# Kernel optimization log

Hardware: AMD Instinct MI355X
Metric: run time of the kernel (lower is better)

Reference implementation:

```python
import jax, jax.numpy as jnp
import numpy as np

NUM_HEADS = 16
EMBED_DIM = 1024
INPUT_DIM = 1024
B, S = 4, 1024
MASK_VAL = -1e30  # fp32 branch of the original code


def setup_inputs() -> dict:
    key = jax.random.key(0)
    k1, k2, k3, k4 = jax.random.split(key, 4)
    x = jax.random.normal(k1, (B, S, INPUT_DIM), dtype=jnp.float32)
    mask = jax.random.randint(k2, (B, S), 0, 2, dtype=jnp.int32)
    # xavier_uniform-like init
    lim_qkv = float(np.sqrt(6.0 / (INPUT_DIM + 3 * EMBED_DIM)))
    lim_out = float(np.sqrt(6.0 / (EMBED_DIM + EMBED_DIM)))
    w_qkv = jax.random.uniform(k3, (3 * EMBED_DIM, INPUT_DIM), jnp.float32, -lim_qkv, lim_qkv)
    b_qkv = jnp.zeros((3 * EMBED_DIM,), jnp.float32)
    w_out = jax.random.uniform(k4, (EMBED_DIM, EMBED_DIM), jnp.float32, -lim_out, lim_out)
    b_out = jnp.zeros((EMBED_DIM,), jnp.float32)
    return {"x": x, "mask": mask, "w_qkv": w_qkv, "b_qkv": b_qkv,
            "w_out": w_out, "b_out": b_out}


def reference(x, mask, w_qkv, b_qkv, w_out, b_out):
    Bz, Sl, _ = x.shape
    Dh = EMBED_DIM // NUM_HEADS
    qkv = x @ w_qkv.T + b_qkv                       # (B,S,3E)
    q, k, v = jnp.split(qkv, 3, axis=-1)
    q = q.reshape(Bz, Sl, NUM_HEADS, Dh).transpose(0, 2, 1, 3)  # (B,H,S,Dh)
    k = k.reshape(Bz, Sl, NUM_HEADS, Dh).transpose(0, 2, 1, 3)
    v = v.reshape(Bz, Sl, NUM_HEADS, Dh).transpose(0, 2, 1, 3)
    energy = jnp.einsum('bhqd,bhkd->bhqk', q, k) / jnp.sqrt(jnp.float32(Dh))
    # Faithful reproduction of the original (buggy-looking) mask semantics:
    # positions with (k <= q) & (q < L_i) & (k < L_i) get filled with -1e30.
    L = mask.sum(axis=-1)                            # (B,)
    idx = jnp.arange(Sl)
    tri = idx[:, None] >= idx[None, :]               # (S,S): k <= q
    valid = idx[None, :] < L[:, None]                # (B,S)
    cond = tri[None, None] & valid[:, None, :, None] & valid[:, None, None, :]
    energy = jnp.where(cond, MASK_VAL, energy)
    attn = jax.nn.softmax(energy, axis=-1)           # (B,H,S,S)
    out = jnp.einsum('bhqk,bhkd->bhqd', attn, v)     # (B,H,S,Dh)
    out = out.transpose(0, 2, 1, 3).reshape(Bz, Sl, EMBED_DIM)
    return out @ w_out.T + b_out
```

## Files before the change

### kernel.cpp

```cpp
#include <hip/hip_runtime.h>


#define NHEADS 16
#define DHEAD  64
#define EDIM   1024
#define SLEN   1024
#define BATCH  4

typedef short bf16x8 __attribute__((ext_vector_type(8)));
typedef float f32x4  __attribute__((ext_vector_type(4)));
typedef float f32x16 __attribute__((ext_vector_type(16)));

#define MFMA_BF16(a,b,c) __builtin_amdgcn_mfma_f32_16x16x32_bf16((a),(b),(c),0,0,0)
#define MFMA32(a,b,c)    __builtin_amdgcn_mfma_f32_32x32x16_bf16((a),(b),(c),0,0,0)

typedef const __attribute__((address_space(1))) void gvoid_t;
typedef __attribute__((address_space(3))) void lvoid_t;

__device__ __forceinline__ unsigned short f2bf(float x) {
  union { float f; unsigned int u; } v; v.f = x;
  unsigned int r = v.u + 0x7fffu + ((v.u >> 16) & 1u);
  return (unsigned short)(r >> 16);
}

__device__ __forceinline__ unsigned pack2(float lo, float hi) {
  return (unsigned)f2bf(lo) | ((unsigned)f2bf(hi) << 16);
}

__device__ __forceinline__ void gl2lds16(const void* g, void* l) {
  __builtin_amdgcn_global_load_lds((gvoid_t*)g, (lvoid_t*)l, 16, 0, 0);
}

__global__ __launch_bounds__(256) void prep_cast(
    const float* __restrict__ x, const float* __restrict__ wq,
    const float* __restrict__ wo,
    unsigned short* __restrict__ xb, unsigned short* __restrict__ wqb,
    unsigned short* __restrict__ wob) {
  int i = blockIdx.x * 256 + threadIdx.x;
  const int NX  = BATCH * SLEN * EDIM / 4;
  const int NW1 = 3 * EDIM * EDIM / 4;
  const float4* src; unsigned short* dst; int j;
  if (i < NX)           { src = (const float4*)x;  dst = xb;  j = i; }
  else if (i < NX+NW1)  { src = (const float4*)wq; dst = wqb; j = i - NX; }
  else                  { src = (const float4*)wo; dst = wob; j = i - NX - NW1; }
  float4 v = src[j];
  ushort4 o;
  o.x = f2bf(v.x); o.y = f2bf(v.y); o.z = f2bf(v.z); o.w = f2bf(v.w);
  ((ushort4*)dst)[j] = o;
}

__global__ __launch_bounds__(256) void mask_sum(const int* __restrict__ mask,
                                                int* __restrict__ L) {
  int b = blockIdx.x;
  int t = threadIdx.x;
  int s = 0;
  for (int i = t; i < SLEN; i += 256) s += mask[b * SLEN + i];
  #pragma unroll
  for (int m = 1; m < 64; m <<= 1) s += __shfl_xor(s, m);
  __shared__ int part[4];
  if ((t & 63) == 0) part[t >> 6] = s;
  __syncthreads();
  if (t == 0) L[b] = part[0] + part[1] + part[2] + part[3];
}

template<int EPI>
__global__ __launch_bounds__(256) void gemm_bt(
    const unsigned short* __restrict__ A, const unsigned short* __restrict__ B,
    int M, int N, int K,
    const float* __restrict__ bias,
    float* __restrict__ outf,
    unsigned short* __restrict__ qb, unsigned short* __restrict__ kb,
    unsigned short* __restrict__ vb) {
  __shared__ __align__(16) unsigned short lds_a[128 * 32];
  __shared__ __align__(16) unsigned short lds_b[128 * 32];
  const int tid = threadIdx.x;
  const int w = tid >> 6, l = tid & 63;
  const int g = l >> 4, ln = l & 15;
  const int ntile = N >> 7;
  const int tm = blockIdx.x / ntile, tn = blockIdx.x % ntile;
  const int mBase = tm << 7, nBase = tn << 7;
  const int wr = w >> 1, wc = w & 1;

  f32x4 zz = {0.f, 0.f, 0.f, 0.f};
  f32x4 acc[4][4];
  #pragma unroll
  for (int m = 0; m < 4; ++m)
    #pragma unroll
    for (int n = 0; n < 4; ++n) acc[m][n] = zz;

  const int u0 = tid, u1 = tid + 256;
  const int r0 = u0 >> 2, c0 = (u0 & 3) << 3;
  const int r1 = u1 >> 2, c1 = (u1 & 3) << 3;
  const unsigned short* Ab = A + mBase * K;
  const unsigned short* Bb = B + nBase * K;
  unsigned short* da0 = &lds_a[(w * 64) * 8];
  unsigned short* da1 = &lds_a[(256 + w * 64) * 8];
  unsigned short* db0 = &lds_b[(w * 64) * 8];
  unsigned short* db1 = &lds_b[(256 + w * 64) * 8];

  for (int k0 = 0; k0 < K; k0 += 32) {
    gl2lds16(Ab + r0 * K + k0 + c0, da0);
    gl2lds16(Ab + r1 * K + k0 + c1, da1);
    gl2lds16(Bb + r0 * K + k0 + c0, db0);
    gl2lds16(Bb + r1 * K + k0 + c1, db1);
    __syncthreads();
    bf16x8 af[4], bfr[4];
    #pragma unroll
    for (int m = 0; m < 4; ++m)
      af[m] = *(const bf16x8*)&lds_a[(wr * 64 + m * 16 + ln) * 32 + g * 8];
    #pragma unroll
    for (int n = 0; n < 4; ++n)
      bfr[n] = *(const bf16x8*)&lds_b[(wc * 64 + n * 16 + ln) * 32 + g * 8];
    #pragma unroll
    for (int m = 0; m < 4; ++m)
      #pragma unroll
      for (int n = 0; n < 4; ++n)
        acc[m][n] = MFMA_BF16(af[m], bfr[n], acc[m][n]);
    __syncthreads();
  }

  #pragma unroll
  for (int m = 0; m < 4; ++m) {
    const int rowb = mBase + wr * 64 + m * 16 + g * 4;
    #pragma unroll
    for (int n = 0; n < 4; ++n) {
      const int col = nBase + wc * 64 + n * 16 + ln;
      const float bv = bias[col];
      #pragma unroll
      for (int r = 0; r < 4; ++r) {
        const float vv = acc[m][n][r] + bv;
        const int row = rowb + r;
        if (EPI == 0) {
          const int part = col >> 10;
          const int c = col & 1023;
          const int hh = c >> 6, d = c & 63;
          const int bb = row >> 10, s = row & 1023;
          const int bh = bb * NHEADS + hh;
          const unsigned short hv = f2bf(vv);
          if (part == 0)      qb[(bh * SLEN + s) * DHEAD + d] = hv;
          else if (part == 1) kb[(bh * SLEN + s) * DHEAD + d] = hv;
          else                vb[(bh * DHEAD + d) * SLEN + s] = hv;
        } else {
          outf[row * N + col] = vv;
        }
      }
    }
  }
}

__global__ __launch_bounds__(256) void attn(
    const unsigned short* __restrict__ qb, const unsigned short* __restrict__ kb,
    const unsigned short* __restrict__ vb, const int* __restrict__ Lp,
    unsigned short* __restrict__ yb) {
  const int bid = blockIdx.x;
  const int lid = (bid & 7) * 256 + (bid >> 3);
  const int bh = lid >> 5, qw = lid & 31;
  const int b = bh >> 4, h = bh & 15;
  const int L = Lp[b];
  const int tid = threadIdx.x;
  const int w = tid >> 6, l = tid & 63;
  const int l31 = l & 31, hi = l >> 5;
  const int q = qw * 32 + l31;

  const unsigned short* qp = qb + (size_t)bh * SLEN * DHEAD;
  const unsigned short* kp = kb + (size_t)bh * SLEN * DHEAD;
  const unsigned short* vp = vb + (size_t)bh * DHEAD * SLEN;

  bf16x8 qf[4];
  #pragma unroll
  for (int c = 0; c < 4; ++c)
    qf[c] = *(const bf16x8*)&qp[q * DHEAD + c * 16 + hi * 8];

  f32x16 o0 = {}; f32x16 o1 = {};
  float mrow = -__builtin_inff(), lrow = 0.f;
  const bool qv = q < L;
  const float C = 0.18033688011112042f;

  const bool allQ  = (qw * 32 + 31) < L;
  const bool noneQ = (qw * 32) >= L;
  const int tstart = (allQ && L < SLEN) ? qw : 0;
  const int tlo = tstart + ((w - tstart) & 3);

  const int tp = tlo < 32 ? tlo : 31;
  bf16x8 kcur[4];
  #pragma unroll
  for (int c = 0; c < 4; ++c)
    kcur[c] = *(const bf16x8*)&kp[(tp * 32 + l31) * DHEAD + c * 16 + hi * 8];

  for (int t = tlo; t < 32; t += 4) {
    const int kb0 = t * 32;
    const int tn = (t + 4 < 32) ? (t + 4) : t;
    bf16x8 knxt[4];
    #pragma unroll
    for (int c = 0; c < 4; ++c)
      knxt[c] = *(const bf16x8*)&kp[(tn * 32 + l31) * DHEAD + c * 16 + hi * 8];
    bf16x8 vf0[2], vf1[2];
    #pragma unroll
    for (int kc = 0; kc < 2; ++kc) {
      vf0[kc] = *(const bf16x8*)&vp[l31 * SLEN + kb0 + kc * 16 + hi * 8];
      vf1[kc] = *(const bf16x8*)&vp[(32 + l31) * SLEN + kb0 + kc * 16 + hi * 8];
    }

    f32x16 e = {};
    __builtin_amdgcn_s_setprio(1);
    #pragma unroll
    for (int c = 0; c < 4; ++c) e = MFMA32(kcur[c], qf[c], e);
    __builtin_amdgcn_s_setprio(0);

    const bool domask = (!noneQ) && (t <= qw);
    float pm = -__builtin_inff();
    if (domask) {
      #pragma unroll
      for (int r = 0; r < 16; ++r) {
        const int key = kb0 + (r & 3) + 8 * (r >> 2) + 4 * hi;
        float s = e[r] * C;
        if (qv && (key <= q)) s = -1e30f;
        e[r] = s;
        pm = fmaxf(pm, s);
      }
    } else {
      #pragma unroll
      for (int r = 0; r < 16; ++r) {
        const float s = e[r] * C;
        e[r] = s;
        pm = fmaxf(pm, s);
      }
    }
    pm = fmaxf(pm, __shfl_xor(pm, 32));

    const bool need = !__all(pm <= mrow + 8.0f);
    if (need) {
      const float mn = fmaxf(mrow, pm);
      const float a = exp2f(mrow - mn);
      #pragma unroll
      for (int r = 0; r < 16; ++r) { o0[r] *= a; o1[r] *= a; }
      lrow *= a;
      mrow = mn;
    }
    float sum = 0.f;
    #pragma unroll
    for (int r = 0; r < 16; ++r) {
      const float pe = exp2f(e[r] - mrow);
      e[r] = pe; sum += pe;
    }
    sum += __shfl_xor(sum, 32);
    lrow += sum;

    bf16x8 pbf[2];
    #pragma unroll
    for (int kc = 0; kc < 2; ++kc) {
      const unsigned wA = pack2(e[8*kc+0], e[8*kc+1]);
      const unsigned wB = pack2(e[8*kc+2], e[8*kc+3]);
      const unsigned wC = pack2(e[8*kc+4], e[8*kc+5]);
      const unsigned wD = pack2(e[8*kc+6], e[8*kc+7]);
      const unsigned pA = __shfl_xor(wA, 32);
      const unsigned pB = __shfl_xor(wB, 32);
      const unsigned pC = __shfl_xor(wC, 32);
      const unsigned pD = __shfl_xor(wD, 32);
      union { unsigned u[4]; bf16x8 v; } pk;
      pk.u[0] = hi ? pC : wA;
      pk.u[1] = hi ? pD : wB;
      pk.u[2] = hi ? wC : pA;
      pk.u[3] = hi ? wD : pB;
      pbf[kc] = pk.v;
    }

    __builtin_amdgcn_s_setprio(1);
    #pragma unroll
    for (int kc = 0; kc < 2; ++kc) {
      o0 = MFMA32(vf0[kc], pbf[kc], o0);
      o1 = MFMA32(vf1[kc], pbf[kc], o1);
    }
    __builtin_amdgcn_s_setprio(0);

    #pragma unroll
    for (int c = 0; c < 4; ++c) kcur[c] = knxt[c];
  }

  __shared__ float mls[4][2][32];
  __shared__ __align__(16) float obuf[2][32][65];
  if (hi == 0) { mls[w][0][l31] = mrow; mls[w][1][l31] = lrow; }
  __syncthreads();
  const float m0 = mls[0][0][l31], m1 = mls[1][0][l31];
  const float m2 = mls[2][0][l31], m3 = mls[3][0][l31];
  const float mstar = fmaxf(fmaxf(m0, m1), fmaxf(m2, m3));
  const float denom = mls[0][1][l31] * exp2f(m0 - mstar)
                    + mls[1][1][l31] * exp2f(m1 - mstar)
                    + mls[2][1][l31] * exp2f(m2 - mstar)
                    + mls[3][1][l31] * exp2f(m3 - mstar);
  const float sw = exp2f(mrow - mstar) / denom;
  #pragma unroll
  for (int r = 0; r < 16; ++r) { o0[r] *= sw; o1[r] *= sw; }
  if (w >= 2) {
    #pragma unroll
    for (int r = 0; r < 16; ++r) {
      const int d = (r & 3) + 8 * (r >> 2) + 4 * hi;
      obuf[w - 2][l31][d]      = o0[r];
      obuf[w - 2][l31][d + 32] = o1[r];
    }
  }
  __syncthreads();
  if (w < 2) {
    #pragma unroll
    for (int r = 0; r < 16; ++r) {
      const int d = (r & 3) + 8 * (r >> 2) + 4 * hi;
      o0[r] += obuf[w][l31][d];
      o1[r] += obuf[w][l31][d + 32];
    }
  }
  __syncthreads();
  if (w == 1) {
    #pragma unroll
    for (int r = 0; r < 16; ++r) {
      const int d = (r & 3) + 8 * (r >> 2) + 4 * hi;
      obuf[0][l31][d]      = o0[r];
      obuf[0][l31][d + 32] = o1[r];
    }
  }
  __syncthreads();
  if (w == 0) {
    #pragma unroll
    for (int r = 0; r < 16; ++r) {
      const int d = (r & 3) + 8 * (r >> 2) + 4 * hi;
      o0[r] += obuf[0][l31][d];
      o1[r] += obuf[0][l31][d + 32];
    }
    unsigned short* yrow = yb + (size_t)(b * SLEN + q) * EDIM + h * DHEAD;
    #pragma unroll
    for (int rq = 0; rq < 4; ++rq) {
      ushort4 s0, s1;
      s0.x = f2bf(o0[4*rq+0]); s0.y = f2bf(o0[4*rq+1]);
      s0.z = f2bf(o0[4*rq+2]); s0.w = f2bf(o0[4*rq+3]);
      s1.x = f2bf(o1[4*rq+0]); s1.y = f2bf(o1[4*rq+1]);
      s1.z = f2bf(o1[4*rq+2]); s1.w = f2bf(o1[4*rq+3]);
      *(ushort4*)&yrow[8*rq + 4*hi]      = s0;
      *(ushort4*)&yrow[32 + 8*rq + 4*hi] = s1;
    }
  }
}

extern "C" void kernel_launch(void* const* d_in, const int* in_sizes, int n_in,
                              void* d_out, int out_size, void* d_ws, size_t ws_size,
                              hipStream_t stream) {
  const float* x    = (const float*)d_in[0];
  const int*   mask = (const int*)d_in[1];
  const float* wqkv = (const float*)d_in[2];
  const float* bqkv = (const float*)d_in[3];
  const float* wout = (const float*)d_in[4];
  const float* bout = (const float*)d_in[5];
  float* out = (float*)d_out;

  char* ws = (char*)d_ws;
  const size_t SZ_X   = (size_t)BATCH * SLEN * EDIM * 2;
  const size_t SZ_WQ  = (size_t)3 * EDIM * EDIM * 2;
  const size_t SZ_WO  = (size_t)EDIM * EDIM * 2;
  const size_t SZ_QKV = (size_t)BATCH * NHEADS * SLEN * DHEAD * 2;

  unsigned short* xb   = (unsigned short*)ws;               ws += SZ_X;
  unsigned short* wqb  = (unsigned short*)ws;               ws += SZ_WQ;
  unsigned short* wob  = (unsigned short*)ws;               ws += SZ_WO;
  unsigned short* qbuf = (unsigned short*)ws;               ws += SZ_QKV;
  unsigned short* kbuf = (unsigned short*)ws;               ws += SZ_QKV;
  unsigned short* vbuf = (unsigned short*)ws;               ws += SZ_QKV;
  unsigned short* ybuf = (unsigned short*)ws;               ws += SZ_X;
  int* Lbuf = (int*)ws;

  prep_cast<<<8192, 256, 0, stream>>>(x, wqkv, wout, xb, wqb, wob);
  mask_sum<<<BATCH, 256, 0, stream>>>(mask, Lbuf);
  gemm_bt<0><<<(4096 / 128) * (3072 / 128), 256, 0, stream>>>(
      xb, wqb, 4096, 3072, 1024, bqkv, nullptr, qbuf, kbuf, vbuf);
  attn<<<BATCH * NHEADS * (SLEN / 32), 256, 0, stream>>>(qbuf, kbuf, vbuf, Lbuf, ybuf);
  gemm_bt<1><<<(4096 / 128) * (1024 / 128), 256, 0, stream>>>(
      ybuf, wob, 4096, 1024, 1024, bout, out, nullptr, nullptr, nullptr);
}
```

Before: 230.4 us.

## Process two 32-query tiles per attention block to reuse K/V loads

Each attention workgroup now handles 64 queries as two 32-row sub-tiles (A and B), sharing each loaded K and V fragment across both sub-tiles' QK and PV MFMAs. The grid halves, and global K/V traffic per query is halved. The cost is doubled accumulator and register state per wave, larger shared-memory reduction buffers, and a combined start tile that may add iterations for the lower sub-tile. Occupancy may drop because of register pressure.

```diff
diff --git a/kernel.cpp b/kernel.cpp
--- a/kernel.cpp
+++ b/kernel.cpp
@@ -153,33 +153,39 @@
     const unsigned short* __restrict__ vb, const int* __restrict__ Lp,
     unsigned short* __restrict__ yb) {
   const int bid = blockIdx.x;
-  const int lid = (bid & 7) * 256 + (bid >> 3);
-  const int bh = lid >> 5, qw = lid & 31;
+  const int lid = (bid & 7) * 128 + (bid >> 3);
+  const int bh = lid >> 4, qp = lid & 15;
   const int b = bh >> 4, h = bh & 15;
   const int L = Lp[b];
   const int tid = threadIdx.x;
   const int w = tid >> 6, l = tid & 63;
   const int l31 = l & 31, hi = l >> 5;
-  const int q = qw * 32 + l31;
-
-  const unsigned short* qp = qb + (size_t)bh * SLEN * DHEAD;
-  const unsigned short* kp = kb + (size_t)bh * SLEN * DHEAD;
-  const unsigned short* vp = vb + (size_t)bh * DHEAD * SLEN;
-
-  bf16x8 qf[4];
+  const int q0 = qp * 64;
+  const int qA = q0 + l31, qB = q0 + 32 + l31;
+  const int qwA = 2 * qp, qwB = 2 * qp + 1;
+
+  const unsigned short* qp_ = qb + (size_t)bh * SLEN * DHEAD;
+  const unsigned short* kp  = kb + (size_t)bh * SLEN * DHEAD;
+  const unsigned short* vp  = vb + (size_t)bh * DHEAD * SLEN;
+
+  bf16x8 qfA[4], qfB[4];
   #pragma unroll
-  for (int c = 0; c < 4; ++c)
-    qf[c] = *(const bf16x8*)&qp[q * DHEAD + c * 16 + hi * 8];
-
-  f32x16 o0 = {}; f32x16 o1 = {};
-  float mrow = -__builtin_inff(), lrow = 0.f;
-  const bool qv = q < L;
+  for (int c = 0; c < 4; ++c) {
+    qfA[c] = *(const bf16x8*)&qp_[qA * DHEAD + c * 16 + hi * 8];
+    qfB[c] = *(const bf16x8*)&qp_[qB * DHEAD + c * 16 + hi * 8];
+  }
+
+  f32x16 o0A = {}, o1A = {}, o0B = {}, o1B = {};
+  float mA = -__builtin_inff(), lsA = 0.f;
+  float mB = -__builtin_inff(), lsB = 0.f;
   const float C = 0.18033688011112042f;
 
-  const bool allQ  = (qw * 32 + 31) < L;
-  const bool noneQ = (qw * 32) >= L;
-  const int tstart = (allQ && L < SLEN) ? qw : 0;
-  const int tlo = tstart + ((w - tstart) & 3);
+  const bool noneA = q0 >= L,        noneB = (q0 + 32) >= L;
+  const bool allA  = (q0 + 31) < L,  allB  = (q0 + 63) < L;
+  const int tsA = (allA && L < SLEN) ? qwA : 0;
+  const int tsB = (allB && L < SLEN) ? qwB : 0;
+  const int ts  = tsA < tsB ? tsA : tsB;
+  const int tlo = ts + ((w - ts) & 3);
 
   const int tp = tlo < 32 ? tlo : 31;
   bf16x8 kcur[4];
@@ -187,6 +193,67 @@
   for (int c = 0; c < 4; ++c)
     kcur[c] = *(const bf16x8*)&kp[(tp * 32 + l31) * DHEAD + c * 16 + hi * 8];
 
+#define SM_PV(SUF)                                                          \
+  {                                                                         \
+    const bool domask = (!none##SUF) && (t <= qw##SUF);                     \
+    float pm = -__builtin_inff();                                           \
+    if (domask) {                                                           \
+      _Pragma("unroll")                                                     \
+      for (int r = 0; r < 16; ++r) {                                        \
+        const int key = kb0 + (r & 3) + 8 * (r >> 2) + 4 * hi;              \
+        float s = e##SUF[r] * C;                                            \
+        if ((q##SUF < L) && (key <= q##SUF)) s = -1e30f;                    \
+        e##SUF[r] = s; pm = fmaxf(pm, s);                                   \
+      }                                                                     \
+    } else {                                                                \
+      _Pragma("unroll")                                                     \
+      for (int r = 0; r < 16; ++r) {                                        \
+        const float s = e##SUF[r] * C; e##SUF[r] = s; pm = fmaxf(pm, s);    \
+      }                                                                     \
+    }                                                                       \
+    pm = fmaxf(pm, __shfl_xor(pm, 32));                                     \
+    const bool need = !__all(pm <= m##SUF + 8.0f);                          \
+    if (need) {                                                             \
+      const float mn = fmaxf(m##SUF, pm);                                   \
+      const float a = exp2f(m##SUF - mn);                                   \
+      _Pragma("unroll")                                                     \
+      for (int r = 0; r < 16; ++r) { o0##SUF[r] *= a; o1##SUF[r] *= a; }    \
+      ls##SUF *= a; m##SUF = mn;                                            \
+    }                                                                       \
+    float sum = 0.f;                                                        \
+    _Pragma("unroll")                                                       \
+    for (int r = 0; r < 16; ++r) {                                          \
+      const float pe = exp2f(e##SUF[r] - m##SUF);                           \
+      e##SUF[r] = pe; sum += pe;                                            \
+    }                                                                       \
+    sum += __shfl_xor(sum, 32);                                             \
+    ls##SUF += sum;                                                         \
+    bf16x8 pbf[2];                                                          \
+    _Pragma("unroll")                                                       \
+    for (int kc = 0; kc < 2; ++kc) {                                        \
+      const unsigned wA_ = pack2(e##SUF[8*kc+0], e##SUF[8*kc+1]);           \
+      const unsigned wB_ = pack2(e##SUF[8*kc+2], e##SUF[8*kc+3]);           \
+      const unsigned wC_ = pack2(e##SUF[8*kc+4], e##SUF[8*kc+5]);           \
+      const unsigned wD_ = pack2(e##SUF[8*kc+6], e##SUF[8*kc+7]);           \
+      const unsigned pA_ = __shfl_xor(wA_, 32);                             \
+      const unsigned pB_ = __shfl_xor(wB_, 32);                             \
+      const unsigned pC_ = __shfl_xor(wC_, 32);                             \
+      const unsigned pD_ = __shfl_xor(wD_, 32);                             \
+      union { unsigned u[4]; bf16x8 v; } pk;                                \
+      pk.u[0] = hi ? pC_ : wA_;                                             \
+      pk.u[1] = hi ? pD_ : wB_;                                             \
+      pk.u[2] = hi ? wC_ : pA_;                                             \
+      pk.u[3] = hi ? wD_ : pB_;                                             \
+      pbf[kc] = pk.v;                                                       \
+    }                                                                       \
+    __builtin_amdgcn_s_setprio(1);                                          \
+    o0##SUF = MFMA32(vf0[0], pbf[0], o0##SUF);                              \
+    o1##SUF = MFMA32(vf1[0], pbf[0], o1##SUF);                              \
+    o0##SUF = MFMA32(vf0[1], pbf[1], o0##SUF);                              \
+    o1##SUF = MFMA32(vf1[1], pbf[1], o1##SUF);                              \
+    __builtin_amdgcn_s_setprio(0);                                          \
+  }
+
   for (int t = tlo; t < 32; t += 4) {
     const int kb0 = t * 32;
     const int tn = (t + 4 < 32) ? (t + 4) : t;
@@ -201,102 +268,59 @@
       vf1[kc] = *(const bf16x8*)&vp[(32 + l31) * SLEN + kb0 + kc * 16 + hi * 8];
     }
 
-    f32x16 e = {};
+    f32x16 eA = {}, eB = {};
     __builtin_amdgcn_s_setprio(1);
     #pragma unroll
-    for (int c = 0; c < 4; ++c) e = MFMA32(kcur[c], qf[c], e);
+    for (int c = 0; c < 4; ++c) eA = MFMA32(kcur[c], qfA[c], eA);
+    #pragma unroll
+    for (int c = 0; c < 4; ++c) eB = MFMA32(kcur[c], qfB[c], eB);
     __builtin_amdgcn_s_setprio(0);
 
-    const bool domask = (!noneQ) && (t <= qw);
-    float pm = -__builtin_inff();
-    if (domask) {
-      #pragma unroll
-      for (int r = 0; r < 16; ++r) {
-        const int key = kb0 + (r & 3) + 8 * (r >> 2) + 4 * hi;
-        float s = e[r] * C;
-        if (qv && (key <= q)) s = -1e30f;
-        e[r] = s;
-        pm = fmaxf(pm, s);
-      }
-    } else {
-      #pragma unroll
-      for (int r = 0; r < 16; ++r) {
-        const float s = e[r] * C;
-        e[r] = s;
-        pm = fmaxf(pm, s);
-      }
-    }
-    pm = fmaxf(pm, __shfl_xor(pm, 32));
-
-    const bool need = !__all(pm <= mrow + 8.0f);
-    if (need) {
-      const float mn = fmaxf(mrow, pm);
-      const float a = exp2f(mrow - mn);
-      #pragma unroll
-      for (int r = 0; r < 16; ++r) { o0[r] *= a; o1[r] *= a; }
-      lrow *= a;
-      mrow = mn;
-    }
-    float sum = 0.f;
-    #pragma unroll
-    for (int r = 0; r < 16; ++r) {
-      const float pe = exp2f(e[r] - mrow);
-      e[r] = pe; sum += pe;
-    }
-    sum += __shfl_xor(sum, 32);
-    lrow += sum;
-
-    bf16x8 pbf[2];
-    #pragma unroll
-    for (int kc = 0; kc < 2; ++kc) {
-      const unsigned wA = pack2(e[8*kc+0], e[8*kc+1]);
-      const unsigned wB = pack2(e[8*kc+2], e[8*kc+3]);
-      const unsigned wC = pack2(e[8*kc+4], e[8*kc+5]);
-      const unsigned wD = pack2(e[8*kc+6], e[8*kc+7]);
-      const unsigned pA = __shfl_xor(wA, 32);
-      const unsigned pB = __shfl_xor(wB, 32);
-      const unsigned pC = __shfl_xor(wC, 32);
-      const unsigned pD = __shfl_xor(wD, 32);
-      union { unsigned u[4]; bf16x8 v; } pk;
-      pk.u[0] = hi ? pC : wA;
-      pk.u[1] = hi ? pD : wB;
-      pk.u[2] = hi ? wC : pA;
-      pk.u[3] = hi ? wD : pB;
-      pbf[kc] = pk.v;
-    }
-
-    __builtin_amdgcn_s_setprio(1);
-    #pragma unroll
-    for (int kc = 0; kc < 2; ++kc) {
-      o0 = MFMA32(vf0[kc], pbf[kc], o0);
-      o1 = MFMA32(vf1[kc], pbf[kc], o1);
-    }
-    __builtin_amdgcn_s_setprio(0);
+    if (t >= tsA) SM_PV(A)
+    if (t >= tsB) SM_PV(B)
 
     #pragma unroll
     for (int c = 0; c < 4; ++c) kcur[c] = knxt[c];
   }
-
-  __shared__ float mls[4][2][32];
-  __shared__ __align__(16) float obuf[2][32][65];
-  if (hi == 0) { mls[w][0][l31] = mrow; mls[w][1][l31] = lrow; }
+#undef SM_PV
+
+  __shared__ float mlsA[4][2][32], mlsB[4][2][32];
+  __shared__ __align__(16) float obufA[2][32][65], obufB[2][32][65];
+  if (hi == 0) {
+    mlsA[w][0][l31] = mA; mlsA[w][1][l31] = lsA;
+    mlsB[w][0][l31] = mB; mlsB[w][1][l31] = lsB;
+  }
   __syncthreads();
-  const float m0 = mls[0][0][l31], m1 = mls[1][0][l31];
-  const float m2 = mls[2][0][l31], m3 = mls[3][0][l31];
-  const float mstar = fmaxf(fmaxf(m0, m1), fmaxf(m2, m3));
-  const float denom = mls[0][1][l31] * exp2f(m0 - mstar)
-                    + mls[1][1][l31] * exp2f(m1 - mstar)
-                    + mls[2][1][l31] * exp2f(m2 - mstar)
-                    + mls[3][1][l31] * exp2f(m3 - mstar);
-  const float sw = exp2f(mrow - mstar) / denom;
-  #pragma unroll
-  for (int r = 0; r < 16; ++r) { o0[r] *= sw; o1[r] *= sw; }
+  {
+    const float a0 = mlsA[0][0][l31], a1 = mlsA[1][0][l31];
+    const float a2 = mlsA[2][0][l31], a3 = mlsA[3][0][l31];
+    const float msA = fmaxf(fmaxf(a0, a1), fmaxf(a2, a3));
+    const float dnA = mlsA[0][1][l31] * exp2f(a0 - msA)
+                    + mlsA[1][1][l31] * exp2f(a1 - msA)
+                    + mlsA[2][1][l31] * exp2f(a2 - msA)
+                    + mlsA[3][1][l31] * exp2f(a3 - msA);
+    const float swA = exp2f(mA - msA) / dnA;
+    #pragma unroll
+    for (int r = 0; r < 16; ++r) { o0A[r] *= swA; o1A[r] *= swA; }
+    const float b0 = mlsB[0][0][l31], b1 = mlsB[1][0][l31];
+    const float b2 = mlsB[2][0][l31], b3 = mlsB[3][0][l31];
+    const float msB = fmaxf(fmaxf(b0, b1), fmaxf(b2, b3));
+    const float dnB = mlsB[0][1][l31] * exp2f(b0 - msB)
+                    + mlsB[1][1][l31] * exp2f(b1 - msB)
+                    + mlsB[2][1][l31] * exp2f(b2 - msB)
+                    + mlsB[3][1][l31] * exp2f(b3 - msB);
+    const float swB = exp2f(mB - msB) / dnB;
+    #pragma unroll
+    for (int r = 0; r < 16; ++r) { o0B[r] *= swB; o1B[r] *= swB; }
+  }
   if (w >= 2) {
     #pragma unroll
     for (int r = 0; r < 16; ++r) {
       const int d = (r & 3) + 8 * (r >> 2) + 4 * hi;
-      obuf[w - 2][l31][d]      = o0[r];
-      obuf[w - 2][l31][d + 32] = o1[r];
+      obufA[w - 2][l31][d]      = o0A[r];
+      obufA[w - 2][l31][d + 32] = o1A[r];
+      obufB[w - 2][l31][d]      = o0B[r];
+      obufB[w - 2][l31][d + 32] = o1B[r];
     }
   }
   __syncthreads();
@@ -304,8 +328,10 @@
     #pragma unroll
     for (int r = 0; r < 16; ++r) {
       const int d = (r & 3) + 8 * (r >> 2) + 4 * hi;
-      o0[r] += obuf[w][l31][d];
-      o1[r] += obuf[w][l31][d + 32];
+      o0A[r] += obufA[w][l31][d];
+      o1A[r] += obufA[w][l31][d + 32];
+      o0B[r] += obufB[w][l31][d];
+      o1B[r] += obufB[w][l31][d + 32];
     }
   }
   __syncthreads();
@@ -313,8 +339,10 @@
     #pragma unroll
     for (int r = 0; r < 16; ++r) {
       const int d = (r & 3) + 8 * (r >> 2) + 4 * hi;
-      obuf[0][l31][d]      = o0[r];
-      obuf[0][l31][d + 32] = o1[r];
+      obufA[0][l31][d]      = o0A[r];
+      obufA[0][l31][d + 32] = o1A[r];
+      obufB[0][l31][d]      = o0B[r];
+      obufB[0][l31][d + 32] = o1B[r];
     }
   }
   __syncthreads();
@@ -322,19 +350,28 @@
     #pragma unroll
     for (int r = 0; r < 16; ++r) {
       const int d = (r & 3) + 8 * (r >> 2) + 4 * hi;
-      o0[r] += obuf[0][l31][d];
-      o1[r] += obuf[0][l31][d + 32];
-    }
-    unsigned short* yrow = yb + (size_t)(b * SLEN + q) * EDIM + h * DHEAD;
+      o0A[r] += obufA[0][l31][d];
+      o1A[r] += obufA[0][l31][d + 32];
+      o0B[r] += obufB[0][l31][d];
+      o1B[r] += obufB[0][l31][d + 32];
+    }
+    unsigned short* yrA = yb + (size_t)(b * SLEN + qA) * EDIM + h * DHEAD;
+    unsigned short* yrB = yb + (size_t)(b * SLEN + qB) * EDIM + h * DHEAD;
     #pragma unroll
     for (int rq = 0; rq < 4; ++rq) {
       ushort4 s0, s1;
-      s0.x = f2bf(o0[4*rq+0]); s0.y = f2bf(o0[4*rq+1]);
-      s0.z = f2bf(o0[4*rq+2]); s0.w = f2bf(o0[4*rq+3]);
-      s1.x = f2bf(o1[4*rq+0]); s1.y = f2bf(o1[4*rq+1]);
-      s1.z = f2bf(o1[4*rq+2]); s1.w = f2bf(o1[4*rq+3]);
-      *(ushort4*)&yrow[8*rq + 4*hi]      = s0;
-      *(ushort4*)&yrow[32 + 8*rq + 4*hi] = s1;
+      s0.x = f2bf(o0A[4*rq+0]); s0.y = f2bf(o0A[4*rq+1]);
+      s0.z = f2bf(o0A[4*rq+2]); s0.w = f2bf(o0A[4*rq+3]);
+      s1.x = f2bf(o1A[4*rq+0]); s1.y = f2bf(o1A[4*rq+1]);
+      s1.z = f2bf(o1A[4*rq+2]); s1.w = f2bf(o1A[4*rq+3]);
+      *(ushort4*)&yrA[8*rq + 4*hi]      = s0;
+      *(ushort4*)&yrA[32 + 8*rq + 4*hi] = s1;
+      s0.x = f2bf(o0B[4*rq+0]); s0.y = f2bf(o0B[4*rq+1]);
+      s0.z = f2bf(o0B[4*rq+2]); s0.w = f2bf(o0B[4*rq+3]);
+      s1.x = f2bf(o1B[4*rq+0]); s1.y = f2bf(o1B[4*rq+1]);
+      s1.z = f2bf(o1B[4*rq+2]); s1.w = f2bf(o1B[4*rq+3]);
+      *(ushort4*)&yrB[8*rq + 4*hi]      = s0;
+      *(ushort4*)&yrB[32 + 8*rq + 4*hi] = s1;
     }
   }
 }
@@ -369,7 +406,7 @@
   mask_sum<<<BATCH, 256, 0, stream>>>(mask, Lbuf);
   gemm_bt<0><<<(4096 / 128) * (3072 / 128), 256, 0, stream>>>(
       xb, wqb, 4096, 3072, 1024, bqkv, nullptr, qbuf, kbuf, vbuf);
-  attn<<<BATCH * NHEADS * (SLEN / 32), 256, 0, stream>>>(qbuf, kbuf, vbuf, Lbuf, ybuf);
+  attn<<<BATCH * NHEADS * (SLEN / 64), 256, 0, stream>>>(qbuf, kbuf, vbuf, Lbuf, ybuf);
   gemm_bt<1><<<(4096 / 128) * (1024 / 128), 256, 0, stream>>>(
       ybuf, wob, 4096, 1024, 1024, bout, out, nullptr, nullptr, nullptr);
 }
```

New measurement: 237.0 us. +2.9%, slower.
